# Kernel tuning notes

Hardware: AMD Instinct MI355X
Metric: run time of the kernel (lower is better)

The kernel has to match this reference:

```python
import jax, jax.numpy as jnp
import numpy as np

L, N, D, K = 8, 1024, 2048, 4096

def setup_inputs() -> dict:
    key = jax.random.key(0)
    k1, k2 = jax.random.split(key)
    x = jax.random.normal(k1, (L, N, D), dtype=jnp.float32)
    centroids = jax.random.normal(k2, (L, K, D), dtype=jnp.float32)
    return {"x": x, "centroids": centroids}

def reference(x, centroids):
    # Euclidean distance of every row of x[l] to every centroid in centroids[l]:
    # ||a-b||^2 = ||a||^2 - 2 a.b + ||b||^2, computed as batched GEMM (one per layer,
    # fused into a single einsum) instead of the original per-row Python loop.
    x2 = jnp.sum(x * x, axis=-1)                        # [L, N]
    c2 = jnp.sum(centroids * centroids, axis=-1)        # [L, K]
    xc = jnp.einsum('lnd,lkd->lnk', x, centroids)       # [L, N, K]
    d2 = x2[:, :, None] - 2.0 * xc + c2[:, None, :]
    return jnp.sqrt(jnp.maximum(d2, 1e-12))             # [L, N, K]
```

## Files before the change

kernel.cpp:

```cpp
#include <hip/hip_runtime.h>
#include <hip/hip_bf16.h>


#define L_DIM 8
#define N_DIM 1024
#define D_DIM 2048
#define K_DIM 4096

typedef __bf16 bf16x8 __attribute__((ext_vector_type(8)));
typedef float floatx4 __attribute__((ext_vector_type(4)));


__device__ __forceinline__ unsigned short f2bf_rne(float f) {
    unsigned u = __float_as_uint(f);
    unsigned r = (u + 0x7FFFu + ((u >> 16) & 1u)) >> 16;
    return (unsigned short)r;
}

__device__ __forceinline__ void lds_cp16(const unsigned short* g, unsigned short* l) {
    __builtin_amdgcn_global_load_lds(
        (const __attribute__((address_space(1))) void*)g,
        (__attribute__((address_space(3))) void*)l,
        16, 0, 0);
}

__global__ __launch_bounds__(256) void prep_kernel(const float* __restrict__ src,
                                                   unsigned short* __restrict__ dst,
                                                   float* __restrict__ norms) {
    const int row = blockIdx.x;
    const int t = threadIdx.x;
    const size_t base = (size_t)row * D_DIM + (size_t)t * 8;

    float4 f0 = *(const float4*)(src + base);
    float4 f1 = *(const float4*)(src + base + 4);

    union { unsigned short us[8]; int4 v; } pk;
    pk.us[0] = f2bf_rne(f0.x); pk.us[1] = f2bf_rne(f0.y);
    pk.us[2] = f2bf_rne(f0.z); pk.us[3] = f2bf_rne(f0.w);
    pk.us[4] = f2bf_rne(f1.x); pk.us[5] = f2bf_rne(f1.y);
    pk.us[6] = f2bf_rne(f1.z); pk.us[7] = f2bf_rne(f1.w);
    *(int4*)(dst + base) = pk.v;

    float s = f0.x*f0.x + f0.y*f0.y + f0.z*f0.z + f0.w*f0.w
            + f1.x*f1.x + f1.y*f1.y + f1.z*f1.z + f1.w*f1.w;
    #pragma unroll
    for (int off = 32; off > 0; off >>= 1) s += __shfl_down(s, off, 64);

    __shared__ float red[4];
    if ((t & 63) == 0) red[t >> 6] = s;
    __syncthreads();
    if (t == 0) norms[row] = red[0] + red[1] + red[2] + red[3];
}

__global__ __launch_bounds__(256) void gemm_mfma(const unsigned short* __restrict__ xb,
                                                 const unsigned short* __restrict__ cb,
                                                 const float* __restrict__ x2,
                                                 const float* __restrict__ c2,
                                                 float* __restrict__ out) {
    __shared__ unsigned short As[128 * 64];
    __shared__ unsigned short Bs[128 * 64];

    const int l  = blockIdx.z;
    const int nb = blockIdx.y;
    const int kb = blockIdx.x;

    const unsigned short* xA = xb + (size_t)l * N_DIM * D_DIM + (size_t)(nb * 128) * D_DIM;
    const unsigned short* cB = cb + (size_t)l * K_DIM * D_DIM + (size_t)(kb * 128) * D_DIM;

    const int t    = threadIdx.x;
    const int wave = t >> 6;
    const int lane = t & 63;
    const int quad = lane >> 4;
    const int lr   = lane & 15;
    const int wr   = (wave >> 1) * 64;
    const int wc   = (wave & 1) * 64;

    floatx4 acc[4][4];
    const floatx4 zero = {0.f, 0.f, 0.f, 0.f};
    #pragma unroll
    for (int i = 0; i < 4; i++)
        #pragma unroll
        for (int j = 0; j < 4; j++) acc[i][j] = zero;

    for (int d0 = 0; d0 < D_DIM; d0 += 64) {
        #pragma unroll
        for (int i = 0; i < 4; i++) {
            const int id  = i * 256 + t;
            const int row = id >> 3;
            const int cc  = id & 7;
            const int ldsbase = (i * 256 + wave * 64) * 8;
            lds_cp16(xA + (size_t)row * D_DIM + d0 + cc * 8, &As[ldsbase]);
            lds_cp16(cB + (size_t)row * D_DIM + d0 + cc * 8, &Bs[ldsbase]);
        }
        __syncthreads();

        #pragma unroll
        for (int ks = 0; ks < 2; ks++) {
            bf16x8 a[4], b[4];
            #pragma unroll
            for (int im = 0; im < 4; im++)
                a[im] = *(const bf16x8*)&As[(wr + im * 16 + lr) * 64 + ks * 32 + quad * 8];
            #pragma unroll
            for (int jn = 0; jn < 4; jn++)
                b[jn] = *(const bf16x8*)&Bs[(wc + jn * 16 + lr) * 64 + ks * 32 + quad * 8];
            #pragma unroll
            for (int im = 0; im < 4; im++)
                #pragma unroll
                for (int jn = 0; jn < 4; jn++)
                    acc[im][jn] = __builtin_amdgcn_mfma_f32_16x16x32_bf16(
                        a[im], b[jn], acc[im][jn], 0, 0, 0);
        }
        __syncthreads();
    }

    const float* x2l = x2 + l * N_DIM + nb * 128;
    const float* c2l = c2 + l * K_DIM + kb * 128;
    float* outl = out + (size_t)l * N_DIM * K_DIM + (size_t)(nb * 128) * K_DIM + kb * 128;

    #pragma unroll
    for (int im = 0; im < 4; im++) {
        const int rbase = wr + im * 16 + quad * 4;
        #pragma unroll
        for (int jn = 0; jn < 4; jn++) {
            const int col = wc + jn * 16 + lr;
            const float c2v = c2l[col];
            #pragma unroll
            for (int r = 0; r < 4; r++) {
                const int row = rbase + r;
                const float d2 = x2l[row] - 2.0f * acc[im][jn][r] + c2v;
                outl[(size_t)row * K_DIM + col] = sqrtf(fmaxf(d2, 1e-12f));
            }
        }
    }
}

__global__ __launch_bounds__(256) void fallback_dist(const float* __restrict__ x,
                                                     const float* __restrict__ c,
                                                     float* __restrict__ out) {
    __shared__ float As[64][33];
    __shared__ float Bs[64][33];
    const int l = blockIdx.z, nb = blockIdx.y, kb = blockIdx.x;
    const float* xA = x + (size_t)l * N_DIM * D_DIM + (size_t)(nb * 64) * D_DIM;
    const float* cB = c + (size_t)l * K_DIM * D_DIM + (size_t)(kb * 64) * D_DIM;
    const int t = threadIdx.x;
    const int tr = t >> 4, tc = t & 15;
    float acc[4][4] = {};
    for (int d0 = 0; d0 < D_DIM; d0 += 32) {
        #pragma unroll
        for (int i = 0; i < 8; i++) {
            const int id = i * 256 + t;
            const int r = id >> 5, cc = id & 31;
            As[r][cc] = xA[(size_t)r * D_DIM + d0 + cc];
            Bs[r][cc] = cB[(size_t)r * D_DIM + d0 + cc];
        }
        __syncthreads();
        #pragma unroll
        for (int kk = 0; kk < 32; kk++) {
            float av[4], bv[4];
            #pragma unroll
            for (int i = 0; i < 4; i++) av[i] = As[tr * 4 + i][kk];
            #pragma unroll
            for (int j = 0; j < 4; j++) bv[j] = Bs[tc * 4 + j][kk];
            #pragma unroll
            for (int i = 0; i < 4; i++)
                #pragma unroll
                for (int j = 0; j < 4; j++) {
                    const float dxy = av[i] - bv[j];
                    acc[i][j] += dxy * dxy;
                }
        }
        __syncthreads();
    }
    float* o = out + (size_t)l * N_DIM * K_DIM + (size_t)(nb * 64) * K_DIM + kb * 64;
    #pragma unroll
    for (int i = 0; i < 4; i++)
        #pragma unroll
        for (int j = 0; j < 4; j++)
            o[(size_t)(tr * 4 + i) * K_DIM + tc * 4 + j] = sqrtf(fmaxf(acc[i][j], 1e-12f));
}

extern "C" void kernel_launch(void* const* d_in, const int* in_sizes, int n_in,
                              void* d_out, int out_size, void* d_ws, size_t ws_size,
                              hipStream_t stream) {
    const float* x = (const float*)d_in[0];
    const float* c = (const float*)d_in[1];
    float* out = (float*)d_out;

    constexpr size_t X_ELEMS = (size_t)L_DIM * N_DIM * D_DIM;
    constexpr size_t C_ELEMS = (size_t)L_DIM * K_DIM * D_DIM;
    constexpr size_t NEED = X_ELEMS * 2 + C_ELEMS * 2
                          + (size_t)L_DIM * N_DIM * 4 + (size_t)L_DIM * K_DIM * 4;

    if (ws_size >= NEED) {
        unsigned short* xb = (unsigned short*)d_ws;
        unsigned short* cb = xb + X_ELEMS;
        float* x2 = (float*)(cb + C_ELEMS);
        float* c2 = x2 + (size_t)L_DIM * N_DIM;

        prep_kernel<<<L_DIM * N_DIM, 256, 0, stream>>>(x, xb, x2);
        prep_kernel<<<L_DIM * K_DIM, 256, 0, stream>>>(c, cb, c2);
        gemm_mfma<<<dim3(K_DIM / 128, N_DIM / 128, L_DIM), 256, 0, stream>>>(xb, cb, x2, c2, out);
    } else {
        fallback_dist<<<dim3(K_DIM / 64, N_DIM / 64, L_DIM), 256, 0, stream>>>(x, c, out);
    }
}
```

Before: 673.8 us.

## XOR-swizzle GEMM LDS tiles and process one row per wave in prep

The GEMM now places each 16-byte chunk of the global rows at an XOR-permuted position (chunk ^ row&7) inside the LDS tile, and the fragment reads apply the same XOR. This spreads the row-strided bf16x8 reads across LDS banks to remove bank conflicts. Separately, the prep kernel now gives each wave a whole row, which removes the shared-memory reduction and the block barrier and cuts the block count by four. The swizzle must stay consistent between the load and read sides or the results will be wrong.

```diff
diff --git a/kernel.cpp b/kernel.cpp
--- a/kernel.cpp
+++ b/kernel.cpp
@@ -27,29 +27,31 @@
 __global__ __launch_bounds__(256) void prep_kernel(const float* __restrict__ src,
                                                    unsigned short* __restrict__ dst,
                                                    float* __restrict__ norms) {
-    const int row = blockIdx.x;
-    const int t = threadIdx.x;
-    const size_t base = (size_t)row * D_DIM + (size_t)t * 8;
-
-    float4 f0 = *(const float4*)(src + base);
-    float4 f1 = *(const float4*)(src + base + 4);
-
-    union { unsigned short us[8]; int4 v; } pk;
-    pk.us[0] = f2bf_rne(f0.x); pk.us[1] = f2bf_rne(f0.y);
-    pk.us[2] = f2bf_rne(f0.z); pk.us[3] = f2bf_rne(f0.w);
-    pk.us[4] = f2bf_rne(f1.x); pk.us[5] = f2bf_rne(f1.y);
-    pk.us[6] = f2bf_rne(f1.z); pk.us[7] = f2bf_rne(f1.w);
-    *(int4*)(dst + base) = pk.v;
-
-    float s = f0.x*f0.x + f0.y*f0.y + f0.z*f0.z + f0.w*f0.w
-            + f1.x*f1.x + f1.y*f1.y + f1.z*f1.z + f1.w*f1.w;
+    const int wave = threadIdx.x >> 6;
+    const int lane = threadIdx.x & 63;
+    const int row  = blockIdx.x * 4 + wave;
+    const size_t rb = (size_t)row * D_DIM;
+
+    float s = 0.f;
+    #pragma unroll
+    for (int p = 0; p < 4; p++) {
+        const size_t base = rb + (size_t)p * 512 + (size_t)lane * 8;
+        float4 f0 = *(const float4*)(src + base);
+        float4 f1 = *(const float4*)(src + base + 4);
+
+        union { unsigned short us[8]; int4 v; } pk;
+        pk.us[0] = f2bf_rne(f0.x); pk.us[1] = f2bf_rne(f0.y);
+        pk.us[2] = f2bf_rne(f0.z); pk.us[3] = f2bf_rne(f0.w);
+        pk.us[4] = f2bf_rne(f1.x); pk.us[5] = f2bf_rne(f1.y);
+        pk.us[6] = f2bf_rne(f1.z); pk.us[7] = f2bf_rne(f1.w);
+        *(int4*)(dst + base) = pk.v;
+
+        s += f0.x*f0.x + f0.y*f0.y + f0.z*f0.z + f0.w*f0.w
+           + f1.x*f1.x + f1.y*f1.y + f1.z*f1.z + f1.w*f1.w;
+    }
     #pragma unroll
     for (int off = 32; off > 0; off >>= 1) s += __shfl_down(s, off, 64);
-
-    __shared__ float red[4];
-    if ((t & 63) == 0) red[t >> 6] = s;
-    __syncthreads();
-    if (t == 0) norms[row] = red[0] + red[1] + red[2] + red[3];
+    if (lane == 0) norms[row] = s;
 }
 
 __global__ __launch_bounds__(256) void gemm_mfma(const unsigned short* __restrict__ xb,
@@ -72,6 +74,7 @@
     const int lane = t & 63;
     const int quad = lane >> 4;
     const int lr   = lane & 15;
+    const int sw   = lr & 7;
     const int wr   = (wave >> 1) * 64;
     const int wc   = (wave & 1) * 64;
 
@@ -88,9 +91,10 @@
             const int id  = i * 256 + t;
             const int row = id >> 3;
             const int cc  = id & 7;
+            const int gcc = cc ^ (row & 7);
             const int ldsbase = (i * 256 + wave * 64) * 8;
-            lds_cp16(xA + (size_t)row * D_DIM + d0 + cc * 8, &As[ldsbase]);
-            lds_cp16(cB + (size_t)row * D_DIM + d0 + cc * 8, &Bs[ldsbase]);
+            lds_cp16(xA + (size_t)row * D_DIM + d0 + gcc * 8, &As[ldsbase]);
+            lds_cp16(cB + (size_t)row * D_DIM + d0 + gcc * 8, &Bs[ldsbase]);
         }
         __syncthreads();
 
@@ -99,10 +103,10 @@
             bf16x8 a[4], b[4];
             #pragma unroll
             for (int im = 0; im < 4; im++)
-                a[im] = *(const bf16x8*)&As[(wr + im * 16 + lr) * 64 + ks * 32 + quad * 8];
+                a[im] = *(const bf16x8*)&As[(wr + im * 16 + lr) * 64 + ((ks * 4 + quad) ^ sw) * 8];
             #pragma unroll
             for (int jn = 0; jn < 4; jn++)
-                b[jn] = *(const bf16x8*)&Bs[(wc + jn * 16 + lr) * 64 + ks * 32 + quad * 8];
+                b[jn] = *(const bf16x8*)&Bs[(wc + jn * 16 + lr) * 64 + ((ks * 4 + quad) ^ sw) * 8];
             #pragma unroll
             for (int im = 0; im < 4; im++)
                 #pragma unroll
@@ -197,8 +201,8 @@
         float* x2 = (float*)(cb + C_ELEMS);
         float* c2 = x2 + (size_t)L_DIM * N_DIM;
 
-        prep_kernel<<<L_DIM * N_DIM, 256, 0, stream>>>(x, xb, x2);
-        prep_kernel<<<L_DIM * K_DIM, 256, 0, stream>>>(c, cb, c2);
+        prep_kernel<<<L_DIM * N_DIM / 4, 256, 0, stream>>>(x, xb, x2);
+        prep_kernel<<<L_DIM * K_DIM / 4, 256, 0, stream>>>(c, cb, c2);
         gemm_mfma<<<dim3(K_DIM / 128, N_DIM / 128, L_DIM), 256, 0, stream>>>(xb, cb, x2, c2, out);
     } else {
         fallback_dist<<<dim3(K_DIM / 64, N_DIM / 64, L_DIM), 256, 0, stream>>>(x, c, out);
```

After: 652.6 us. -3.1%, faster.
